# Optimization experiments

Hardware: AMD Instinct MI355X
Metric: run time of the kernel (lower is better)

The kernel has to match this reference:

```python
import jax, jax.numpy as jnp
import numpy as np

B, S, D = 1, 2048, 4096
H = 32
Q_RANK, KV_RANK = 1536, 512
NOPE, ROPE, VD = 128, 64, 128
QD = NOPE + ROPE  # 192
EPS = 1e-6
THETA = 10000.0


def setup_inputs() -> dict:
    key = jax.random.key(0)
    ks = jax.random.split(key, 8)
    std = 0.02
    return {
        'hidden_states': jax.random.normal(ks[0], (B, S, D), jnp.float32),
        'Wq_a': jax.random.normal(ks[1], (D, Q_RANK), jnp.float32) * std,
        'q_a_ln_w': jnp.ones((Q_RANK,), jnp.float32),
        'Wq_b': jax.random.normal(ks[2], (Q_RANK, H * QD), jnp.float32) * std,
        'Wkv_a': jax.random.normal(ks[3], (D, KV_RANK + ROPE), jnp.float32) * std,
        'kv_a_ln_w': jnp.ones((KV_RANK,), jnp.float32),
        'Wkv_b': jax.random.normal(ks[4], (KV_RANK, H * (NOPE + VD)), jnp.float32) * std,
        'Wo': jax.random.normal(ks[5], (H * VD, D), jnp.float32) * std,
    }


def _rmsnorm(x, w):
    return x * jax.lax.rsqrt(jnp.mean(x * x, axis=-1, keepdims=True) + EPS) * w


def _rotate_half(x):
    h = x.shape[-1] // 2
    return jnp.concatenate([-x[..., h:], x[..., :h]], axis=-1)


def _apply_rope(x, cos, sin):
    # DeepSeek interleave permutation: view(..., d//2, 2).transpose -> [evens | odds]
    xp = jnp.concatenate([x[..., 0::2], x[..., 1::2]], axis=-1)
    return xp * cos + _rotate_half(xp) * sin


def _mla_forward(hidden_states, Wq_a, q_a_ln_w, Wq_b, Wkv_a, kv_a_ln_w, Wkv_b, Wo):
    b, s, _ = hidden_states.shape
    # low-rank query projection
    q = _rmsnorm(hidden_states @ Wq_a, q_a_ln_w) @ Wq_b          # [b,s,H*QD]
    q = q.reshape(b, s, H, QD).transpose(0, 2, 1, 3)             # [b,H,s,QD]
    q_nope, q_pe = q[..., :NOPE], q[..., NOPE:]
    # compressed kv + shared rope key
    ckv = hidden_states @ Wkv_a                                   # [b,s,KV_RANK+ROPE]
    compressed, k_pe = ckv[..., :KV_RANK], ckv[..., KV_RANK:]
    kv = _rmsnorm(compressed, kv_a_ln_w) @ Wkv_b                 # [b,s,H*(NOPE+VD)]
    kv = kv.reshape(b, s, H, NOPE + VD).transpose(0, 2, 1, 3)    # [b,H,s,NOPE+VD]
    k_nope, v = kv[..., :NOPE], kv[..., NOPE:]
    k_pe = k_pe[:, None, :, :]                                    # [b,1,s,ROPE]
    # rotary tables (cos/sin duplicated halves)
    inv_freq = 1.0 / (THETA ** (jnp.arange(0, ROPE, 2, dtype=jnp.float32) / ROPE))
    freqs = jnp.outer(jnp.arange(s, dtype=jnp.float32), inv_freq)  # [s,ROPE/2]
    emb = jnp.concatenate([freqs, freqs], axis=-1)                 # [s,ROPE]
    cos = jnp.cos(emb)[None, None].astype(hidden_states.dtype)
    sin = jnp.sin(emb)[None, None].astype(hidden_states.dtype)
    q_pe = _apply_rope(q_pe, cos, sin)
    k_pe = _apply_rope(k_pe, cos, sin)
    # assemble full q/k heads
    qf = jnp.concatenate([q_nope, q_pe], axis=-1)                 # [b,H,s,QD]
    kf = jnp.concatenate([k_nope, jnp.broadcast_to(k_pe, (b, H, s, ROPE))], axis=-1)
    scale = QD ** (-0.5)
    scores = jnp.einsum('bhqd,bhkd->bhqk', qf, kf) * scale        # [b,H,s,s]
    causal = jnp.tril(jnp.ones((s, s), dtype=bool))
    scores = jnp.where(causal, scores, jnp.finfo(scores.dtype).min)
    probs = jax.nn.softmax(scores, axis=-1)
    o = jnp.einsum('bhqk,bhkd->bhqd', probs, v)                   # [b,H,s,VD]
    o = o.transpose(0, 2, 1, 3).reshape(b, s, H * VD)
    return o @ Wo


def reference(hidden_states, Wq_a, q_a_ln_w, Wq_b, Wkv_a, kv_a_ln_w, Wkv_b, Wo):
    return _mla_forward(hidden_states, Wq_a, q_a_ln_w, Wq_b, Wkv_a, kv_a_ln_w, Wkv_b, Wo)
```

## Files before the change

### kernel.cpp

```cpp
#include <hip/hip_runtime.h>

typedef unsigned short u16;
using bf16x8 = __attribute__((ext_vector_type(8))) __bf16;
using f32x4  = __attribute__((ext_vector_type(4))) float;
using s16x8  = __attribute__((ext_vector_type(8))) short;
using s16x4  = __attribute__((ext_vector_type(4))) short;

#define AS1 __attribute__((address_space(1)))
#define AS3 __attribute__((address_space(3)))

__device__ __forceinline__ void gload16(const u16* g, u16* l) {
  __builtin_amdgcn_global_load_lds((AS1 void*)(size_t)g, (AS3 void*)l, 16, 0, 0);
}

__device__ __forceinline__ u16 f2bf(float f) {
  unsigned u = __float_as_uint(f);
  u += 0x7fffu + ((u >> 16) & 1u);
  return (u16)(u >> 16);
}
__device__ __forceinline__ float bf2f(u16 h) {
  return __uint_as_float(((unsigned)h) << 16);
}

__global__ __launch_bounds__(256) void cast_bf16_kernel(const float* __restrict__ x,
                                                        u16* __restrict__ y, int n) {
  int i = (blockIdx.x * 256 + threadIdx.x) * 4;
  if (i + 3 < n) {
    float4 v = *reinterpret_cast<const float4*>(x + i);
    s16x4 o;
    o[0] = (short)f2bf(v.x); o[1] = (short)f2bf(v.y);
    o[2] = (short)f2bf(v.z); o[3] = (short)f2bf(v.w);
    *reinterpret_cast<s16x4*>(y + i) = o;
  }
}

__global__ __launch_bounds__(256) void transpose_cast_kernel(const float* __restrict__ W,
                                                             u16* __restrict__ WT,
                                                             int K, int N) {
  __shared__ u16 tile[64][72];
  const int t = threadIdx.x;
  const int nb = blockIdx.x * 64, kb = blockIdx.y * 64;
  const int rr = t >> 3;
  const int cc = (t & 7) * 8;
#pragma unroll
  for (int pass = 0; pass < 2; ++pass) {
    const float* src = W + (size_t)(kb + pass * 32 + rr) * N + nb + cc;
    float4 a = *reinterpret_cast<const float4*>(src);
    float4 b = *reinterpret_cast<const float4*>(src + 4);
    u16* tr = &tile[pass * 32 + rr][cc];
    tr[0] = f2bf(a.x); tr[1] = f2bf(a.y); tr[2] = f2bf(a.z); tr[3] = f2bf(a.w);
    tr[4] = f2bf(b.x); tr[5] = f2bf(b.y); tr[6] = f2bf(b.z); tr[7] = f2bf(b.w);
  }
  __syncthreads();
#pragma unroll
  for (int pass = 0; pass < 2; ++pass) {
    s16x8 v;
#pragma unroll
    for (int j = 0; j < 8; ++j) v[j] = (short)tile[cc + j][pass * 32 + rr];
    *reinterpret_cast<s16x8*>(WT + (size_t)(nb + pass * 32 + rr) * K + kb + cc) = v;
  }
}

__global__ __launch_bounds__(256) void rmsnorm_kernel(const u16* __restrict__ x,
                                                      const float* __restrict__ w,
                                                      u16* __restrict__ y,
                                                      int R, int xs, int ys) {
  const int row = blockIdx.x, t = threadIdx.x;
  const u16* xr = x + (size_t)row * xs;
  float ss = 0.f;
  for (int i = t; i < R; i += 256) { float f = bf2f(xr[i]); ss += f * f; }
#pragma unroll
  for (int m = 32; m >= 1; m >>= 1) ss += __shfl_xor(ss, m);
  __shared__ float red[4];
  if ((t & 63) == 0) red[t >> 6] = ss;
  __syncthreads();
  float tot = red[0] + red[1] + red[2] + red[3];
  float r = rsqrtf(tot / (float)R + 1e-6f);
  u16* yr = y + (size_t)row * ys;
  for (int i = t; i < R; i += 256) yr[i] = f2bf(bf2f(xr[i]) * r * w[i]);
}

__global__ __launch_bounds__(256) void rope_table_kernel(float* __restrict__ cost,
                                                         float* __restrict__ sint) {
  int idx = blockIdx.x * 256 + threadIdx.x;
  int pos = idx >> 5, j = idx & 31;
  float inv = __expf(-(float)j * (9.210340371976184f / 32.0f));
  float f = (float)pos * inv;
  cost[idx] = cosf(f);
  sint[idx] = sinf(f);
}

__global__ __launch_bounds__(256) void build_qf_kernel(const u16* __restrict__ q,
                                                       const float* __restrict__ cost,
                                                       const float* __restrict__ sint,
                                                       u16* __restrict__ qf) {
  int tid = blockIdx.x * 256 + threadIdx.x;
  int o8 = tid * 8;
  if (o8 >= 32 * 2048 * 192) return;
  const float scale = 0.07216878364870323f;
  int c = (o8 % 192) >> 3;
  int rest = o8 / 192;
  int s = rest & 2047, h = rest >> 11;
  const u16* qrow = q + ((size_t)s * 32 + h) * 192;
  s16x8 out;
  if (c < 16) {
    s16x8 v = *reinterpret_cast<const s16x8*>(qrow + c * 8);
#pragma unroll
    for (int j = 0; j < 8; ++j) out[j] = (short)f2bf(bf2f((u16)v[j]) * scale);
  } else {
    int j0 = c * 8 - 128;
    bool lo = j0 < 32;
    int jj0 = lo ? j0 : j0 - 32;
    s16x8 a = *reinterpret_cast<const s16x8*>(qrow + 128 + 2 * jj0);
    s16x8 b = *reinterpret_cast<const s16x8*>(qrow + 128 + 2 * jj0 + 8);
    float4 c0 = *reinterpret_cast<const float4*>(cost + s * 32 + jj0);
    float4 c1 = *reinterpret_cast<const float4*>(cost + s * 32 + jj0 + 4);
    float4 s0 = *reinterpret_cast<const float4*>(sint + s * 32 + jj0);
    float4 s1 = *reinterpret_cast<const float4*>(sint + s * 32 + jj0 + 4);
    float cs[8] = {c0.x, c0.y, c0.z, c0.w, c1.x, c1.y, c1.z, c1.w};
    float sn[8] = {s0.x, s0.y, s0.z, s0.w, s1.x, s1.y, s1.z, s1.w};
#pragma unroll
    for (int j = 0; j < 8; ++j) {
      float x0 = bf2f((u16)((j < 4) ? a[2 * j] : b[2 * j - 8]));
      float x1 = bf2f((u16)((j < 4) ? a[2 * j + 1] : b[2 * j - 7]));
      float v = lo ? (x0 * cs[j] - x1 * sn[j]) : (x1 * cs[j] + x0 * sn[j]);
      out[j] = (short)f2bf(v * scale);
    }
  }
  *reinterpret_cast<s16x8*>(qf + o8) = out;
}

__global__ __launch_bounds__(256) void build_kf_kernel(const u16* __restrict__ kv,
                                                       const u16* __restrict__ ckv,
                                                       const float* __restrict__ cost,
                                                       const float* __restrict__ sint,
                                                       u16* __restrict__ kf) {
  int tid = blockIdx.x * 256 + threadIdx.x;
  int o8 = tid * 8;
  if (o8 >= 32 * 2048 * 192) return;
  int c = (o8 % 192) >> 3;
  int rest = o8 / 192;
  int s = rest & 2047, h = rest >> 11;
  s16x8 out;
  if (c < 16) {
    out = *reinterpret_cast<const s16x8*>(kv + ((size_t)s * 32 + h) * 256 + c * 8);
  } else {
    int j0 = c * 8 - 128;
    bool lo = j0 < 32;
    int jj0 = lo ? j0 : j0 - 32;
    const u16* crow = ckv + (size_t)s * 2112 + 512;
    s16x8 a = *reinterpret_cast<const s16x8*>(crow + 2 * jj0);
    s16x8 b = *reinterpret_cast<const s16x8*>(crow + 2 * jj0 + 8);
    float4 c0 = *reinterpret_cast<const float4*>(cost + s * 32 + jj0);
    float4 c1 = *reinterpret_cast<const float4*>(cost + s * 32 + jj0 + 4);
    float4 s0 = *reinterpret_cast<const float4*>(sint + s * 32 + jj0);
    float4 s1 = *reinterpret_cast<const float4*>(sint + s * 32 + jj0 + 4);
    float cs[8] = {c0.x, c0.y, c0.z, c0.w, c1.x, c1.y, c1.z, c1.w};
    float sn[8] = {s0.x, s0.y, s0.z, s0.w, s1.x, s1.y, s1.z, s1.w};
#pragma unroll
    for (int j = 0; j < 8; ++j) {
      float x0 = bf2f((u16)((j < 4) ? a[2 * j] : b[2 * j - 8]));
      float x1 = bf2f((u16)((j < 4) ? a[2 * j + 1] : b[2 * j - 7]));
      float v = lo ? (x0 * cs[j] - x1 * sn[j]) : (x1 * cs[j] + x0 * sn[j]);
      out[j] = (short)f2bf(v);
    }
  }
  *reinterpret_cast<s16x8*>(kf + o8) = out;
}

__global__ __launch_bounds__(256) void vt_build_kernel(const u16* __restrict__ kv,
                                                       u16* __restrict__ vT) {
  __shared__ u16 tile[64][72];
  const int t = threadIdx.x;
  const int sb = blockIdx.x * 64, db = blockIdx.y * 64, h = blockIdx.z;
  const int rr = t >> 3, cc = (t & 7) * 8;
#pragma unroll
  for (int pass = 0; pass < 2; ++pass) {
    const u16* src = kv + (size_t)(sb + pass * 32 + rr) * 8192 + h * 256 + 128 + db + cc;
    s16x8 v = *reinterpret_cast<const s16x8*>(src);
#pragma unroll
    for (int j = 0; j < 8; ++j) tile[pass * 32 + rr][cc + j] = (u16)v[j];
  }
  __syncthreads();
#pragma unroll
  for (int pass = 0; pass < 2; ++pass) {
    s16x8 v;
#pragma unroll
    for (int j = 0; j < 8; ++j) v[j] = (short)tile[cc + j][pass * 32 + rr];
    *reinterpret_cast<s16x8*>(vT + ((size_t)h * 128 + db + pass * 32 + rr) * 2048 + sb + cc) = v;
  }
}

template <int OUT_BF16>
__global__ __launch_bounds__(256) void gemm_v3_kernel(const u16* __restrict__ A,
                                                      const u16* __restrict__ BT,
                                                      void* __restrict__ Cv,
                                                      int M, int N, int K) {
  __shared__ __align__(16) u16 S[4 * 8192];
  const int t0 = threadIdx.x;
  const int lane = t0 & 63, wave = t0 >> 6;
  const int wr = wave >> 1, wc = wave & 1;
  const int row0 = blockIdx.y * 128, col0 = blockIdx.x * 128;
  const int lrow = lane & 15, lkg = lane >> 4;

  const int lp = lane ^ ((lane >> 3) & 3);
  const int srow_off = lp >> 2;
  const int skel = (lp & 3) * 8;
  const int c0 = wave * 2, c1 = c0 + 1;
  const int arow_c0 = row0 + c0 * 16 + srow_off;
  const int arow_c1 = row0 + c1 * 16 + srow_off;
  int brow_c0 = col0 + c0 * 16 + srow_off; if (brow_c0 > N - 1) brow_c0 = N - 1;
  int brow_c1 = col0 + c1 * 16 + srow_off; if (brow_c1 > N - 1) brow_c1 = N - 1;

  int aoff[4], boff[4];
#pragma unroll
  for (int m = 0; m < 4; ++m) {
    int r = wr * 64 + m * 16 + lrow;
    int off = r * 32 + lkg * 8;
    aoff[m] = off ^ ((off >> 3) & 0x18);
    r = wc * 64 + m * 16 + lrow;
    off = r * 32 + lkg * 8;
    boff[m] = off ^ ((off >> 3) & 0x18);
  }

  const int NT = K >> 5;

#pragma unroll
  for (int pt = 0; pt < 3; ++pt) {
    u16* ab = &S[pt * 8192];
    const int kb = pt * 32 + skel;
    gload16(A  + (size_t)arow_c0 * K + kb, ab + c0 * 512);
    gload16(A  + (size_t)arow_c1 * K + kb, ab + c1 * 512);
    gload16(BT + (size_t)brow_c0 * K + kb, ab + 4096 + c0 * 512);
    gload16(BT + (size_t)brow_c1 * K + kb, ab + 4096 + c1 * 512);
  }

  f32x4 acc[4][4];
#pragma unroll
  for (int m = 0; m < 4; ++m)
#pragma unroll
    for (int n = 0; n < 4; ++n) acc[m][n] = 0.f;

  for (int t = 0; t < NT; ++t) {
    if (t + 2 < NT)      asm volatile("s_waitcnt vmcnt(8)" ::: "memory");
    else if (t + 1 < NT) asm volatile("s_waitcnt vmcnt(4)" ::: "memory");
    else                 asm volatile("s_waitcnt vmcnt(0)" ::: "memory");
    __builtin_amdgcn_s_barrier();
    __builtin_amdgcn_sched_barrier(0);

    const u16* ab = &S[(t & 3) * 8192];
    bf16x8 af[4], bb[4];
#pragma unroll
    for (int m = 0; m < 4; ++m)
      af[m] = *reinterpret_cast<const bf16x8*>(ab + aoff[m]);
#pragma unroll
    for (int n = 0; n < 4; ++n)
      bb[n] = *reinterpret_cast<const bf16x8*>(ab + 4096 + boff[n]);

    if (t + 3 < NT) {
      u16* sb = &S[((t + 3) & 3) * 8192];
      const int kb = (t + 3) * 32 + skel;
      gload16(A  + (size_t)arow_c0 * K + kb, sb + c0 * 512);
      gload16(A  + (size_t)arow_c1 * K + kb, sb + c1 * 512);
      gload16(BT + (size_t)brow_c0 * K + kb, sb + 4096 + c0 * 512);
      gload16(BT + (size_t)brow_c1 * K + kb, sb + 4096 + c1 * 512);
    }

    __builtin_amdgcn_s_setprio(1);
#pragma unroll
    for (int m = 0; m < 4; ++m)
#pragma unroll
      for (int n = 0; n < 4; ++n)
        acc[m][n] = __builtin_amdgcn_mfma_f32_16x16x32_bf16(af[m], bb[n], acc[m][n], 0, 0, 0);
    __builtin_amdgcn_s_setprio(0);
  }

#pragma unroll
  for (int m = 0; m < 4; ++m) {
#pragma unroll
    for (int n = 0; n < 4; ++n) {
      int col = col0 + wc * 64 + n * 16 + lrow;
      if (col < N) {
#pragma unroll
        for (int i = 0; i < 4; ++i) {
          int row = row0 + wr * 64 + m * 16 + lkg * 4 + i;
          size_t idx = (size_t)row * N + col;
          if (OUT_BF16) ((u16*)Cv)[idx] = f2bf(acc[m][n][i]);
          else          ((float*)Cv)[idx] = acc[m][n][i];
        }
      }
    }
  }
}

__global__ __launch_bounds__(256) void mla_attn_kernel(const u16* __restrict__ qf,
                                                       const u16* __restrict__ kf,
                                                       const u16* __restrict__ vT,
                                                       u16* __restrict__ o) {
  const int h = blockIdx.x, qb = 15 - blockIdx.y;
  const int t = threadIdx.x, wave = t >> 6, lane = t & 63;
  const int lrow = lane & 15, lkg = lane >> 4;
  __shared__ __align__(16) u16 Kt[24 * 512];
  __shared__ __align__(16) u16 Vt[16 * 512];
  __shared__ __align__(16) u16 Pl[4][32][72];

  const u16* ksrc0 = kf + ((size_t)h * 2048 + wave * 16 + lrow) * 192 + lkg * 8;
  const u16* vsrc0 = vT + ((size_t)h * 128 + wave * 32 + lrow) * 2048 + lkg * 8;

  const int qbase = qb * 128 + wave * 32;

  bf16x8 qfr[2][6];
#pragma unroll
  for (int r = 0; r < 2; ++r) {
    const u16* qp = qf + ((size_t)h * 2048 + qbase + r * 16 + lrow) * 192 + lkg * 8;
#pragma unroll
    for (int kk = 0; kk < 6; ++kk)
      qfr[r][kk] = *reinterpret_cast<const bf16x8*>(qp + kk * 32);
  }

  f32x4 acc[2][8];
#pragma unroll
  for (int r = 0; r < 2; ++r)
#pragma unroll
    for (int f = 0; f < 8; ++f) acc[r][f] = 0.f;
  float m_run[2][4], l_par[2][4];
#pragma unroll
  for (int r = 0; r < 2; ++r)
#pragma unroll
    for (int i = 0; i < 4; ++i) { m_run[r][i] = -1e30f; l_par[r][i] = 0.f; }

  const int kv_end = qb * 128 + 128;
  for (int kt = 0; kt < kv_end; kt += 64) {
    {
      const u16* ks = ksrc0 + (size_t)kt * 192;
#pragma unroll
      for (int kk = 0; kk < 6; ++kk)
        gload16(ks + kk * 32, &Kt[(wave * 6 + kk) * 512]);
#pragma unroll
      for (int j = 0; j < 4; ++j) {
        int fo = (j >> 1), ck = j & 1;
        gload16(vsrc0 + (size_t)fo * 16 * 2048 + kt + ck * 32,
                &Vt[((wave * 2 + fo) * 2 + ck) * 512]);
      }
    }
    __syncthreads();

    if (kt <= qbase + 31) {
      f32x4 sv[2][4];
#pragma unroll
      for (int r = 0; r < 2; ++r)
#pragma unroll
        for (int cg = 0; cg < 4; ++cg) sv[r][cg] = 0.f;
#pragma unroll
      for (int cg = 0; cg < 4; ++cg)
#pragma unroll
        for (int kk = 0; kk < 6; ++kk) {
          bf16x8 kfr = *reinterpret_cast<const bf16x8*>(&Kt[(cg * 6 + kk) * 512 + lane * 8]);
          sv[0][cg] = __builtin_amdgcn_mfma_f32_16x16x32_bf16(qfr[0][kk], kfr, sv[0][cg], 0, 0, 0);
          sv[1][cg] = __builtin_amdgcn_mfma_f32_16x16x32_bf16(qfr[1][kk], kfr, sv[1][cg], 0, 0, 0);
        }

      if (kt + 63 > qbase) {
#pragma unroll
        for (int r = 0; r < 2; ++r)
#pragma unroll
          for (int cg = 0; cg < 4; ++cg) {
            int kvcol = kt + cg * 16 + lrow;
            int rowb = qbase + r * 16 + lkg * 4;
#pragma unroll
            for (int i = 0; i < 4; ++i)
              if (kvcol > rowb + i) sv[r][cg][i] = -__builtin_inff();
          }
      }

#pragma unroll
      for (int r = 0; r < 2; ++r) {
        float tmax[4];
#pragma unroll
        for (int i = 0; i < 4; ++i)
          tmax[i] = fmaxf(fmaxf(sv[r][0][i], sv[r][1][i]), fmaxf(sv[r][2][i], sv[r][3][i]));
#pragma unroll
        for (int m = 8; m >= 1; m >>= 1)
#pragma unroll
          for (int i = 0; i < 4; ++i) tmax[i] = fmaxf(tmax[i], __shfl_xor(tmax[i], m));
        int need = 0;
#pragma unroll
        for (int i = 0; i < 4; ++i) need |= (tmax[i] > m_run[r][i] + 8.f) ? 1 : 0;
        if (__any(need)) {
#pragma unroll
          for (int i = 0; i < 4; ++i) {
            float mnew = fmaxf(m_run[r][i], tmax[i]);
            float alpha = __expf(m_run[r][i] - mnew);
            m_run[r][i] = mnew;
            l_par[r][i] *= alpha;
#pragma unroll
            for (int f = 0; f < 8; ++f) acc[r][f][i] *= alpha;
          }
        }
#pragma unroll
        for (int i = 0; i < 4; ++i) {
#pragma unroll
          for (int cg = 0; cg < 4; ++cg) sv[r][cg][i] = __expf(sv[r][cg][i] - m_run[r][i]);
          l_par[r][i] += (sv[r][0][i] + sv[r][1][i]) + (sv[r][2][i] + sv[r][3][i]);
        }
#pragma unroll
        for (int cg = 0; cg < 4; ++cg)
#pragma unroll
          for (int i = 0; i < 4; ++i)
            Pl[wave][r * 16 + lkg * 4 + i][cg * 16 + lrow] = f2bf(sv[r][cg][i]);
      }

#pragma unroll
      for (int ck = 0; ck < 2; ++ck) {
        bf16x8 pf0 = *reinterpret_cast<const bf16x8*>(&Pl[wave][lrow][ck * 32 + lkg * 8]);
        bf16x8 pf1 = *reinterpret_cast<const bf16x8*>(&Pl[wave][16 + lrow][ck * 32 + lkg * 8]);
#pragma unroll
        for (int f = 0; f < 8; ++f) {
          bf16x8 vfr = *reinterpret_cast<const bf16x8*>(&Vt[(f * 2 + ck) * 512 + lane * 8]);
          acc[0][f] = __builtin_amdgcn_mfma_f32_16x16x32_bf16(pf0, vfr, acc[0][f], 0, 0, 0);
          acc[1][f] = __builtin_amdgcn_mfma_f32_16x16x32_bf16(pf1, vfr, acc[1][f], 0, 0, 0);
        }
      }
    }
    __syncthreads();
  }

#pragma unroll
  for (int r = 0; r < 2; ++r)
#pragma unroll
    for (int i = 0; i < 4; ++i)
#pragma unroll
      for (int m = 8; m >= 1; m >>= 1) l_par[r][i] += __shfl_xor(l_par[r][i], m);
#pragma unroll
  for (int r = 0; r < 2; ++r)
#pragma unroll
    for (int f = 0; f < 8; ++f)
#pragma unroll
      for (int i = 0; i < 4; ++i) {
        int row = qbase + r * 16 + lkg * 4 + i;
        int col = h * 128 + f * 16 + lrow;
        o[(size_t)row * 4096 + col] = f2bf(acc[r][f][i] / l_par[r][i]);
      }
}

extern "C" void kernel_launch(void* const* d_in, const int* in_sizes, int n_in,
                              void* d_out, int out_size, void* d_ws, size_t ws_size,
                              hipStream_t stream) {
  (void)in_sizes; (void)n_in; (void)out_size; (void)ws_size;
  const float* hs   = (const float*)d_in[0];
  const float* Wqa  = (const float*)d_in[1];
  const float* qln  = (const float*)d_in[2];
  const float* Wqb  = (const float*)d_in[3];
  const float* Wkva = (const float*)d_in[4];
  const float* kvln = (const float*)d_in[5];
  const float* Wkvb = (const float*)d_in[6];
  const float* Wo   = (const float*)d_in[7];
  float* out = (float*)d_out;

  char* p = (char*)d_ws;
  size_t off = 0;
  auto carve = [&](size_t bytes) {
    char* r = p + off;
    off += (bytes + 255) & ~(size_t)255;
    return r;
  };
  u16* hs_bf = (u16*)carve((size_t)2048 * 4096 * 2);
  u16* WabT  = (u16*)carve((size_t)2112 * 4096 * 2);
  u16* WqbT  = (u16*)carve((size_t)6144 * 1536 * 2);
  u16* WkvbT = (u16*)carve((size_t)8192 * 512 * 2);
  u16* WoT   = (u16*)carve((size_t)4096 * 4096 * 2);
  u16* fused = (u16*)carve((size_t)2048 * 2112 * 2);
  u16* qan   = (u16*)carve((size_t)2048 * 1536 * 2);
  u16* q     = (u16*)carve((size_t)2048 * 6144 * 2);
  u16* cn    = (u16*)carve((size_t)2048 * 512 * 2);
  u16* kv    = (u16*)carve((size_t)2048 * 8192 * 2);
  u16* qfb   = (u16*)carve((size_t)32 * 2048 * 192 * 2);
  u16* kfb   = (u16*)carve((size_t)32 * 2048 * 192 * 2);
  u16* vTb   = (u16*)carve((size_t)32 * 128 * 2048 * 2);
  u16* ob    = (u16*)carve((size_t)2048 * 4096 * 2);
  float* cost = (float*)carve((size_t)65536 * 4);
  float* sint = (float*)carve((size_t)65536 * 4);

  cast_bf16_kernel<<<8192, 256, 0, stream>>>(hs, hs_bf, 2048 * 4096);
  transpose_cast_kernel<<<dim3(24, 64), 256, 0, stream>>>(Wqa, WabT, 4096, 1536);
  transpose_cast_kernel<<<dim3(9, 64), 256, 0, stream>>>(Wkva, WabT + (size_t)1536 * 4096, 4096, 576);
  transpose_cast_kernel<<<dim3(96, 24), 256, 0, stream>>>(Wqb, WqbT, 1536, 6144);
  transpose_cast_kernel<<<dim3(128, 8), 256, 0, stream>>>(Wkvb, WkvbT, 512, 8192);
  transpose_cast_kernel<<<dim3(64, 64), 256, 0, stream>>>(Wo, WoT, 4096, 4096);
  rope_table_kernel<<<256, 256, 0, stream>>>(cost, sint);

  gemm_v3_kernel<1><<<dim3(17, 16), 256, 0, stream>>>(hs_bf, WabT, fused, 2048, 2112, 4096);

  rmsnorm_kernel<<<2048, 256, 0, stream>>>(fused, qln, qan, 1536, 2112, 1536);
  rmsnorm_kernel<<<2048, 256, 0, stream>>>(fused + 1536, kvln, cn, 512, 2112, 512);

  gemm_v3_kernel<1><<<dim3(48, 16), 256, 0, stream>>>(qan, WqbT, q, 2048, 6144, 1536);
  gemm_v3_kernel<1><<<dim3(64, 16), 256, 0, stream>>>(cn, WkvbT, kv, 2048, 8192, 512);

  build_qf_kernel<<<6144, 256, 0, stream>>>(q, cost, sint, qfb);
  build_kf_kernel<<<6144, 256, 0, stream>>>(kv, fused + 1536, cost, sint, kfb);
  vt_build_kernel<<<dim3(32, 2, 32), 256, 0, stream>>>(kv, vTb);

  mla_attn_kernel<<<dim3(32, 16), 256, 0, stream>>>(qfb, kfb, vTb, ob);

  gemm_v3_kernel<0><<<dim3(32, 16), 256, 0, stream>>>(ob, WoT, out, 2048, 4096, 4096);
}
```

Baseline: 461.9 us.

## Double-buffer K/V tiles and widen attention blocks to 8 waves

The attention kernel now uses 512-thread blocks covering 256 query rows, with K and V tiles double-buffered in LDS. Each iteration prefetches the next tile via global_load_lds and waits with a partial vmcnt, so loads overlap compute. Each 64-key tile is now shared by 8 waves instead of 4, halving K/V loads per query row. Costs: LDS roughly doubles, there are fewer blocks (256), and the load schedule is hand-tuned with s_waitcnt. The forward block order (qb = blockIdx.y) may also change how the causal workload balances across CUs.

New measurement: 468.2 us. No clear change (+1.4%).

```diff
diff --git a/kernel.cpp b/kernel.cpp
--- a/kernel.cpp
+++ b/kernel.cpp
@@ -293,21 +293,37 @@
   }
 }
 
-__global__ __launch_bounds__(256) void mla_attn_kernel(const u16* __restrict__ qf,
-                                                       const u16* __restrict__ kf,
-                                                       const u16* __restrict__ vT,
-                                                       u16* __restrict__ o) {
-  const int h = blockIdx.x, qb = 15 - blockIdx.y;
+__global__ __launch_bounds__(512, 2) void mla_attn_kernel(const u16* __restrict__ qf,
+                                                          const u16* __restrict__ kf,
+                                                          const u16* __restrict__ vT,
+                                                          u16* __restrict__ o) {
+  const int h = blockIdx.x, qb = blockIdx.y;
   const int t = threadIdx.x, wave = t >> 6, lane = t & 63;
   const int lrow = lane & 15, lkg = lane >> 4;
-  __shared__ __align__(16) u16 Kt[24 * 512];
-  __shared__ __align__(16) u16 Vt[16 * 512];
-  __shared__ __align__(16) u16 Pl[4][32][72];
-
-  const u16* ksrc0 = kf + ((size_t)h * 2048 + wave * 16 + lrow) * 192 + lkg * 8;
-  const u16* vsrc0 = vT + ((size_t)h * 128 + wave * 32 + lrow) * 2048 + lkg * 8;
-
-  const int qbase = qb * 128 + wave * 32;
+  __shared__ __align__(16) u16 Kt[2][24 * 512];
+  __shared__ __align__(16) u16 Vt[2][16 * 512];
+  __shared__ __align__(16) u16 Pl[8][32][72];
+
+  const u16* src0[5]; int step[5]; u16 *dst0[5], *dst1[5];
+#pragma unroll
+  for (int i = 0; i < 5; ++i) {
+    int c = wave * 5 + i;
+    if (c < 24) {
+      int cg = c / 6, kk = c - cg * 6;
+      src0[i] = kf + ((size_t)h * 2048 + cg * 16 + lrow) * 192 + kk * 32 + lkg * 8;
+      step[i] = 192;
+      dst0[i] = &Kt[0][(cg * 6 + kk) * 512];
+      dst1[i] = &Kt[1][(cg * 6 + kk) * 512];
+    } else {
+      int j = c - 24, f = j >> 1, ck = j & 1;
+      src0[i] = vT + ((size_t)h * 128 + f * 16 + lrow) * 2048 + ck * 32 + lkg * 8;
+      step[i] = 1;
+      dst0[i] = &Vt[0][(f * 2 + ck) * 512];
+      dst1[i] = &Vt[1][(f * 2 + ck) * 512];
+    }
+  }
+
+  const int qbase = qb * 256 + wave * 32;
 
   bf16x8 qfr[2][6];
 #pragma unroll
@@ -329,22 +345,28 @@
 #pragma unroll
     for (int i = 0; i < 4; ++i) { m_run[r][i] = -1e30f; l_par[r][i] = 0.f; }
 
-  const int kv_end = qb * 128 + 128;
-  for (int kt = 0; kt < kv_end; kt += 64) {
-    {
-      const u16* ks = ksrc0 + (size_t)kt * 192;
-#pragma unroll
-      for (int kk = 0; kk < 6; ++kk)
-        gload16(ks + kk * 32, &Kt[(wave * 6 + kk) * 512]);
-#pragma unroll
-      for (int j = 0; j < 4; ++j) {
-        int fo = (j >> 1), ck = j & 1;
-        gload16(vsrc0 + (size_t)fo * 16 * 2048 + kt + ck * 32,
-                &Vt[((wave * 2 + fo) * 2 + ck) * 512]);
-      }
-    }
-    __syncthreads();
-
+  const int nt = qb * 4 + 4;
+
+#pragma unroll
+  for (int i = 0; i < 5; ++i) gload16(src0[i], dst0[i]);
+
+  for (int it = 0; it < nt; ++it) {
+    const int kt = it * 64;
+    if (it + 1 < nt) {
+      const size_t adv = (size_t)(kt + 64);
+      const int nb = (it + 1) & 1;
+#pragma unroll
+      for (int i = 0; i < 5; ++i)
+        gload16(src0[i] + adv * step[i], nb ? dst1[i] : dst0[i]);
+      asm volatile("s_waitcnt vmcnt(5)" ::: "memory");
+    } else {
+      asm volatile("s_waitcnt vmcnt(0)" ::: "memory");
+    }
+    __builtin_amdgcn_s_barrier();
+    __builtin_amdgcn_sched_barrier(0);
+
+    const u16* Kb = &Kt[it & 1][0];
+    const u16* Vb = &Vt[it & 1][0];
     if (kt <= qbase + 31) {
       f32x4 sv[2][4];
 #pragma unroll
@@ -355,7 +377,7 @@
       for (int cg = 0; cg < 4; ++cg)
 #pragma unroll
         for (int kk = 0; kk < 6; ++kk) {
-          bf16x8 kfr = *reinterpret_cast<const bf16x8*>(&Kt[(cg * 6 + kk) * 512 + lane * 8]);
+          bf16x8 kfr = *reinterpret_cast<const bf16x8*>(&Kb[(cg * 6 + kk) * 512 + lane * 8]);
           sv[0][cg] = __builtin_amdgcn_mfma_f32_16x16x32_bf16(qfr[0][kk], kfr, sv[0][cg], 0, 0, 0);
           sv[1][cg] = __builtin_amdgcn_mfma_f32_16x16x32_bf16(qfr[1][kk], kfr, sv[1][cg], 0, 0, 0);
         }
@@ -416,13 +438,14 @@
         bf16x8 pf1 = *reinterpret_cast<const bf16x8*>(&Pl[wave][16 + lrow][ck * 32 + lkg * 8]);
 #pragma unroll
         for (int f = 0; f < 8; ++f) {
-          bf16x8 vfr = *reinterpret_cast<const bf16x8*>(&Vt[(f * 2 + ck) * 512 + lane * 8]);
+          bf16x8 vfr = *reinterpret_cast<const bf16x8*>(&Vb[(f * 2 + ck) * 512 + lane * 8]);
           acc[0][f] = __builtin_amdgcn_mfma_f32_16x16x32_bf16(pf0, vfr, acc[0][f], 0, 0, 0);
           acc[1][f] = __builtin_amdgcn_mfma_f32_16x16x32_bf16(pf1, vfr, acc[1][f], 0, 0, 0);
         }
       }
     }
-    __syncthreads();
+    __builtin_amdgcn_sched_barrier(0);
+    __builtin_amdgcn_s_barrier();
   }
 
 #pragma unroll
@@ -501,7 +524,7 @@
   build_kf_kernel<<<6144, 256, 0, stream>>>(kv, fused + 1536, cost, sint, kfb);
   vt_build_kernel<<<dim3(32, 2, 32), 256, 0, stream>>>(kv, vTb);
 
-  mla_attn_kernel<<<dim3(32, 16), 256, 0, stream>>>(qfb, kfb, vTb, ob);
+  mla_attn_kernel<<<dim3(32, 8), 512, 0, stream>>>(qfb, kfb, vTb, ob);
 
   gemm_v3_kernel<0><<<dim3(32, 16), 256, 0, stream>>>(ob, WoT, out, 2048, 4096, 4096);
 }
```
